# Performance work log

Measured on AMD Instinct MI355X. Metric: run time of the kernel, lower is better.

## Reference

```python
import jax, jax.numpy as jnp
import numpy as np
import math

B, S, D, H = 4, 4096, 1024, 128

def setup_inputs() -> dict:
    key = jax.random.key(0)
    ks = jax.random.split(key, 4)
    scale = 1.0 / math.sqrt(D)
    return {
        "inputs": jax.random.normal(ks[0], (B, S, D), dtype=jnp.float32),
        "Wk": jax.random.normal(ks[1], (H, D), dtype=jnp.float32) * scale,
        "bk": jnp.zeros((H,), dtype=jnp.float32),
        "Wq": jax.random.normal(ks[2], (H, D), dtype=jnp.float32) * scale,
        "bq": jnp.zeros((H,), dtype=jnp.float32),
        "Wv": jax.random.normal(ks[3], (H, D), dtype=jnp.float32) * scale,
        "bv": jnp.zeros((H,), dtype=jnp.float32),
        "padding_mask": jnp.ones((B, S), dtype=jnp.int32),
    }

def reference(inputs, Wk, bk, Wq, bq, Wv, bv, padding_mask):
    # Linear projections: [B,S,D] x [H,D]^T -> [B,S,H]
    k = jnp.einsum('bsd,hd->bsh', inputs, Wk) + bk
    q = jnp.einsum('bsd,hd->bsh', inputs, Wq) + bq
    v = jnp.einsum('bsd,hd->bsh', inputs, Wv) + bv
    # Scaled dot-product scores: [B,S,S]
    scores = jnp.einsum('bqh,bkh->bqk', q, k) / jnp.sqrt(jnp.float32(k.shape[-1]))
    # Mask out padded key positions (mask==0 -> -1e9), broadcast over query dim
    scores = jnp.where(padding_mask[:, None, :] == 0, jnp.float32(-1e9), scores)
    weights = jax.nn.softmax(scores, axis=-1)
    # Dropout is identity in eval mode (reference runs inference / training=False)
    out = jnp.einsum('bqk,bkh->bqh', weights, v)
    return out
```

## Files before the change

kernel.cpp:

```cpp
#include <hip/hip_runtime.h>
#include <cmath>

#define B_ 4
#define S_ 4096
#define D_ 1024
#define H_ 128
#define M_ (B_*S_)
#define NQT 32

typedef _Float16 half8 __attribute__((ext_vector_type(8)));
typedef _Float16 half4 __attribute__((ext_vector_type(4)));
typedef float f32x4 __attribute__((ext_vector_type(4)));
typedef float f32x16 __attribute__((ext_vector_type(16)));
typedef int i32x4 __attribute__((ext_vector_type(4)));

#define LOG2E 1.44269504088896340f

__device__ __forceinline__ void gload16(const void* g, void* l) {
    __builtin_amdgcn_global_load_lds(
        (const __attribute__((address_space(1))) unsigned int*)g,
        (__attribute__((address_space(3))) unsigned int*)l,
        16, 0, 0);
}

__global__ __launch_bounds__(256) void conv_w(
    const float* __restrict__ Wq, const float* __restrict__ Wk,
    const float* __restrict__ Wv, _Float16* __restrict__ wh)
{
    const int idx  = blockIdx.x * 256 + threadIdx.x;
    const int base = idx * 8;
    const int m    = base >> 17;
    const int off  = base & ((H_ * D_) - 1);
    const float* src = (m == 0 ? Wq : m == 1 ? Wk : Wv) + off;
    const float4 a = ((const float4*)src)[0];
    const float4 c = ((const float4*)src)[1];
    half8 h = { (_Float16)a.x, (_Float16)a.y, (_Float16)a.z, (_Float16)a.w,
                (_Float16)c.x, (_Float16)c.y, (_Float16)c.z, (_Float16)c.w };
    *(half8*)(wh + base) = h;
}

__global__ __launch_bounds__(256, 3) void proj_kernel(
    const float* __restrict__ x, const _Float16* __restrict__ wh,
    const float* __restrict__ bq, const float* __restrict__ bk,
    const float* __restrict__ bv,
    _Float16* __restrict__ qh, _Float16* __restrict__ kh,
    _Float16* __restrict__ vt)
{
    __shared__ _Float16 Xs[2][64][72];
    __shared__ _Float16 Ws2[2][128][64];

    const int t = threadIdx.x;
    const int yb = blockIdx.y;
    const float* __restrict__ bias = (yb == 0) ? bq : (yb == 1) ? bk : bv;
    const int m0 = blockIdx.x * 64;
    const int w = t >> 6, lane = t & 63;
    const int lg = lane >> 4, lr = lane & 15;

    f32x4 acc[8];
    #pragma unroll
    for (int i = 0; i < 8; ++i) acc[i] = f32x4{0.f, 0.f, 0.f, 0.f};

    const int xrow = t >> 2, xc = (t & 3) * 16;
    const float* xbase = x + (size_t)(m0 + xrow) * D_ + xc;

    int wbyte[4];
    #pragma unroll
    for (int i = 0; i < 4; ++i) {
        const int wrow = 32 * w + 8 * i + (lane >> 3);
        const int wblk = (lane & 7) ^ (lane >> 3);
        wbyte[i] = (wrow * D_ + wblk * 8) * 2;
    }
    const char* whb = (const char*)(wh + (size_t)yb * H_ * D_);

    float4 xfA[4], xfB[4];

#define WISSUE(KT, BUF)                                                       \
    {                                                                         \
        const char* wsrc = whb + (KT) * (64 * 2);                             \
        _Pragma("unroll")                                                     \
        for (int i = 0; i < 4; ++i)                                           \
            gload16(wsrc + wbyte[i], &Ws2[BUF][32 * w + 8 * i][0]);           \
    }
#define XISSUE(KT, XS)                                                        \
    {                                                                         \
        const float4* xs_ = (const float4*)(xbase + (KT) * 64);               \
        _Pragma("unroll") for (int i = 0; i < 4; ++i) XS[i] = xs_[i];         \
    }
#define XWRITE(XS, BUF)                                                       \
    {                                                                         \
        _Pragma("unroll") for (int i = 0; i < 4; ++i) {                       \
            half4 h = { (_Float16)XS[i].x, (_Float16)XS[i].y,                 \
                        (_Float16)XS[i].z, (_Float16)XS[i].w };               \
            *(half4*)&Xs[BUF][xrow][xc + 4 * i] = h;                          \
        }                                                                     \
    }
#define PMFMA(BUF)                                                            \
    {                                                                         \
        _Pragma("unroll") for (int kk = 0; kk < 2; ++kk) {                    \
            half8 a = *(const half8*)&Xs[BUF][w * 16 + lr][kk * 32 + 8 * lg]; \
            _Pragma("unroll") for (int ni = 0; ni < 8; ++ni) {                \
                half8 bfr = *(const half8*)&Ws2[BUF][ni * 16 + lr]            \
                                [((4 * kk + lg) ^ (lr & 7)) * 8];             \
                acc[ni] = __builtin_amdgcn_mfma_f32_16x16x32_f16(a, bfr, acc[ni], 0, 0, 0); \
            }                                                                 \
        }                                                                     \
    }

    WISSUE(0, 0)
    XISSUE(0, xfA)
    XISSUE(1, xfB)
    XWRITE(xfA, 0)
    __syncthreads();

    for (int kt = 0; kt < 16; kt += 2) {
        WISSUE(kt + 1, 1)
        if (kt + 2 < 16) XISSUE(kt + 2, xfA)
        PMFMA(0)
        XWRITE(xfB, 1)
        __syncthreads();
        if (kt + 2 < 16) WISSUE(kt + 2, 0)
        if (kt + 3 < 16) XISSUE(kt + 3, xfB)
        PMFMA(1)
        if (kt + 2 < 16) XWRITE(xfA, 0)
        __syncthreads();
    }
#undef WISSUE
#undef XISSUE
#undef XWRITE
#undef PMFMA

    const float qscale = 0.08838834764831845f * LOG2E;
    const int rowb = m0 + w * 16 + lg * 4;
    #pragma unroll
    for (int ni = 0; ni < 8; ++ni) {
        const int col = ni * 16 + lr;
        const float bval = bias[col];
        if (yb == 0) {
            #pragma unroll
            for (int r = 0; r < 4; ++r)
                qh[(size_t)(rowb + r) * H_ + col] = (_Float16)((acc[ni][r] + bval) * qscale);
        } else if (yb == 1) {
            #pragma unroll
            for (int r = 0; r < 4; ++r)
                kh[(size_t)(rowb + r) * H_ + col] = (_Float16)(acc[ni][r] + bval);
        } else {
            const int bb = rowb >> 12, s0 = rowb & (S_ - 1);
            half4 h;
            #pragma unroll
            for (int r = 0; r < 4; ++r) h[r] = (_Float16)(acc[ni][r] + bval);
            *(half4*)&vt[(size_t)bb * H_ * S_ + (size_t)col * S_ + s0] = h;
        }
    }
}

__device__ __forceinline__ void attn_tile32(
    const _Float16 (&Kb)[64][128], const _Float16 (&Vb)[128][64],
    const half8 (&qf)[8], f32x16 (&acc2)[4], float& m_, float& l_,
    int muse, int lane)
{
    const unsigned long long bz = __ballot(muse == 0);
    const int l31 = lane & 31, l7 = lane & 7, hi = lane >> 5;

    f32x16 sf[2];
    #pragma unroll
    for (int nb = 0; nb < 2; ++nb)
        #pragma unroll
        for (int r = 0; r < 16; ++r) sf[nb][r] = 0.f;
    __builtin_amdgcn_s_setprio(1);
    #pragma unroll
    for (int kt = 0; kt < 8; ++kt) {
        #pragma unroll
        for (int nb = 0; nb < 2; ++nb) {
            half8 kb = *(const half8*)&Kb[nb * 32 + l31][((2 * kt + hi) ^ l7) * 8];
            sf[nb] = __builtin_amdgcn_mfma_f32_32x32x16_f16(kb, qf[kt], sf[nb], 0, 0, 0);
        }
    }
    __builtin_amdgcn_s_setprio(0);
    if (bz) {
        #pragma unroll
        for (int nb = 0; nb < 2; ++nb)
            #pragma unroll
            for (int r = 0; r < 16; ++r) {
                const int kv = nb * 32 + (r & 3) + 8 * (r >> 2) + 4 * hi;
                if ((bz >> kv) & 1ull) sf[nb][r] = -3e9f;
            }
    }
    float tv[16];
    #pragma unroll
    for (int r = 0; r < 16; ++r) tv[r] = fmaxf(sf[0][r], sf[1][r]);
    #pragma unroll
    for (int off = 8; off > 0; off >>= 1)
        #pragma unroll
        for (int r = 0; r < off; ++r) tv[r] = fmaxf(tv[r], tv[r + off]);
    float tmax = fmaxf(tv[0], __shfl_xor(tv[0], 32));
    if (!__all(tmax <= m_ + 8.f)) {
        const float mn  = fmaxf(m_, tmax);
        const float scl = exp2f(m_ - mn);
        m_ = mn; l_ *= scl;
        #pragma unroll
        for (int hb = 0; hb < 4; ++hb) acc2[hb] *= scl;
    }
    #pragma unroll
    for (int nb = 0; nb < 2; ++nb)
        #pragma unroll
        for (int r = 0; r < 16; ++r) sf[nb][r] = exp2f(sf[nb][r] - m_);
    float sv[16];
    #pragma unroll
    for (int r = 0; r < 16; ++r) sv[r] = sf[0][r] + sf[1][r];
    #pragma unroll
    for (int off = 8; off > 0; off >>= 1)
        #pragma unroll
        for (int r = 0; r < off; ++r) sv[r] += sv[r + off];
    l_ += sv[0] + __shfl_xor(sv[0], 32);

    int pkw[2][8];
    #pragma unroll
    for (int nb = 0; nb < 2; ++nb)
        #pragma unroll
        for (int i = 0; i < 8; ++i) {
            auto h2 = __builtin_amdgcn_cvt_pkrtz(sf[nb][2 * i], sf[nb][2 * i + 1]);
            pkw[nb][i] = __builtin_bit_cast(int, h2);
        }
    #pragma unroll
    for (int nb = 0; nb < 2; ++nb)
        #pragma unroll
        for (int hf = 0; hf < 2; ++hf) {
            const int i0 = hf * 4;
            const int sA = hi ? pkw[nb][i0 + 0] : pkw[nb][i0 + 2];
            const int sB = hi ? pkw[nb][i0 + 1] : pkw[nb][i0 + 3];
            const int rA = __shfl_xor(sA, 32);
            const int rB = __shfl_xor(sB, 32);
            const int n0 = hi ? rA : pkw[nb][i0 + 0];
            const int n1 = hi ? rB : pkw[nb][i0 + 1];
            const int n2 = hi ? pkw[nb][i0 + 2] : rA;
            const int n3 = hi ? pkw[nb][i0 + 3] : rB;
            pkw[nb][i0 + 0] = n0; pkw[nb][i0 + 1] = n1;
            pkw[nb][i0 + 2] = n2; pkw[nb][i0 + 3] = n3;
        }
    __builtin_amdgcn_s_setprio(1);
    #pragma unroll
    for (int s = 0; s < 4; ++s) {
        const int nb = s >> 1, hf = s & 1;
        const half8 pb = __builtin_bit_cast(half8,
            i32x4{ pkw[nb][hf * 4 + 0], pkw[nb][hf * 4 + 1],
                   pkw[nb][hf * 4 + 2], pkw[nb][hf * 4 + 3] });
        #pragma unroll
        for (int hb = 0; hb < 4; ++hb) {
            half8 vb = *(const half8*)&Vb[hb * 32 + l31][((2 * s + hi) ^ l7) * 8];
            acc2[hb] = __builtin_amdgcn_mfma_f32_32x32x16_f16(vb, pb, acc2[hb], 0, 0, 0);
        }
    }
    __builtin_amdgcn_s_setprio(0);
}

__global__ __launch_bounds__(256, 2) void attn_kernel(
    const _Float16* __restrict__ qh, const _Float16* __restrict__ kh,
    const _Float16* __restrict__ vt, const int* __restrict__ mask,
    float* __restrict__ pout, float* __restrict__ pm, float* __restrict__ pl,
    const int nsplit)
{
    __shared__ _Float16 Ks[2][64][128];
    __shared__ _Float16 Vs[2][128][64];

    const int t = threadIdx.x;
    const int id = blockIdx.x;
    int qt, sp, b;
    const int ncombo = B_ * nsplit;
    if ((ncombo & 7) == 0) {
        const int per_xcd = ncombo >> 3;
        const int j = id >> 3;
        qt = j & (NQT - 1);
        const int combo = (id & 7) * per_xcd + (j >> 5);
        sp = combo % nsplit; b = combo / nsplit;
    } else {
        qt = id & (NQT - 1);
        const int rest = id >> 5;
        sp = rest % nsplit; b = rest / nsplit;
    }
    const int q0 = qt * 128;
    const int w = t >> 6, lane = t & 63;
    const int l31 = lane & 31, hi = lane >> 5;
    const int kvlen  = S_ / nsplit;
    const int iters  = kvlen >> 6;
    const int kvbase = sp * kvlen;

    int kbyte[4], vbyte[4];
    #pragma unroll
    for (int i = 0; i < 4; ++i) {
        const int krow = 16 * w + 4 * i + (lane >> 4);
        const int kblk = (lane & 15) ^ (krow & 7);
        kbyte[i] = (krow * H_ + kblk * 8) * 2;
        const int vrow = 32 * w + 8 * i + (lane >> 3);
        const int vblk = (lane & 7) ^ (lane >> 3);
        vbyte[i] = (vrow * S_ + vblk * 8) * 2;
    }
    const char* kbase_b = (const char*)(kh + (size_t)(b * S_ + kvbase) * H_);
    const char* vbase_b = (const char*)(vt + (size_t)b * H_ * S_ + kvbase);
    const char* mbase_b = (const char*)(mask + b * S_ + kvbase + lane);

#define ISSUE_TILE(IT, NB, MRECV)                                             \
    {                                                                         \
        const char* kb_t = kbase_b + (size_t)(IT) * (64 * H_ * 2);            \
        const char* vb_t = vbase_b + (size_t)(IT) * (64 * 2);                 \
        _Pragma("unroll")                                                     \
        for (int i = 0; i < 4; ++i)                                           \
            gload16(kb_t + kbyte[i], &Ks[NB][16 * w + 4 * i][0]);             \
        _Pragma("unroll")                                                     \
        for (int i = 0; i < 4; ++i)                                           \
            gload16(vb_t + vbyte[i], &Vs[NB][32 * w + 8 * i][0]);             \
        MRECV = *(const int*)(mbase_b + (size_t)(IT) * 256);                  \
    }
#define WAIT9  asm volatile("s_waitcnt vmcnt(9)" ::: "memory")
#define WAIT0  asm volatile("s_waitcnt vmcnt(0)" ::: "memory")
#define BAR    asm volatile("s_barrier" ::: "memory")

    half8 qf[8];
    {
        const _Float16* qp = qh + (size_t)(b * S_ + q0 + 32 * w + l31) * H_ + 8 * hi;
        #pragma unroll
        for (int kt = 0; kt < 8; ++kt) qf[kt] = *(const half8*)(qp + 16 * kt);
    }

    float m_ = -1e30f, l_ = 0.f;
    f32x16 acc2[4];
    #pragma unroll
    for (int hb = 0; hb < 4; ++hb)
        #pragma unroll
        for (int r = 0; r < 16; ++r) acc2[hb][r] = 0.f;

    int mA, mB;
    ISSUE_TILE(0, 0, mA)
    ISSUE_TILE(1, 1, mB)
    WAIT9;
    BAR;

    for (int it = 0; it < iters; it += 2) {
        attn_tile32(Ks[0], Vs[0], qf, acc2, m_, l_, mA, lane);
        BAR;
        if (it + 2 < iters) { ISSUE_TILE(it + 2, 0, mA) WAIT9; }
        else                { WAIT0; }
        BAR;
        attn_tile32(Ks[1], Vs[1], qf, acc2, m_, l_, mB, lane);
        BAR;
        if (it + 3 < iters) { ISSUE_TILE(it + 3, 1, mB) WAIT9; }
        else                { WAIT0; }
        BAR;
    }
#undef ISSUE_TILE
#undef WAIT9
#undef WAIT0
#undef BAR

    const int qrow = b * S_ + q0 + 32 * w + l31;
    float* op = pout + (size_t)(sp * M_ + qrow) * H_;
    #pragma unroll
    for (int hb = 0; hb < 4; ++hb)
        #pragma unroll
        for (int i = 0; i < 8; ++i) {
            const int h = hb * 32 + 2 * (i & 1) + 8 * (i >> 1) + 4 * hi;
            float2 v2 = make_float2(acc2[hb][2 * i], acc2[hb][2 * i + 1]);
            *(float2*)(op + h) = v2;
        }
    if (hi == 0) {
        pm[sp * M_ + qrow] = m_;
        pl[sp * M_ + qrow] = l_;
    }
}

__global__ __launch_bounds__(256) void combine_kernel(
    const float* __restrict__ pout, const float* __restrict__ pm,
    const float* __restrict__ pl, float* __restrict__ out, const int nsplit)
{
    const int idx = blockIdx.x * 256 + threadIdx.x;
    const int row = idx >> 7;
    const int h   = idx & (H_ - 1);
    float M = -1e30f;
    for (int sp = 0; sp < nsplit; ++sp) M = fmaxf(M, pm[sp * M_ + row]);
    float Z = 0.f, o = 0.f;
    for (int sp = 0; sp < nsplit; ++sp) {
        const float wgt = exp2f(pm[sp * M_ + row] - M);
        Z += wgt * pl[sp * M_ + row];
        o += wgt * pout[(size_t)(sp * M_ + row) * H_ + h];
    }
    out[idx] = o / Z;
}

extern "C" void kernel_launch(void* const* d_in, const int* in_sizes, int n_in,
                              void* d_out, int out_size, void* d_ws, size_t ws_size,
                              hipStream_t stream)
{
    (void)in_sizes; (void)n_in; (void)out_size;
    const float* x  = (const float*)d_in[0];
    const float* Wk = (const float*)d_in[1];
    const float* bk = (const float*)d_in[2];
    const float* Wq = (const float*)d_in[3];
    const float* bq = (const float*)d_in[4];
    const float* Wv = (const float*)d_in[5];
    const float* bv = (const float*)d_in[6];
    const int* mask = (const int*)d_in[7];

    char* ws = (char*)d_ws;
    const size_t qkvBytes = (size_t)M_ * H_ * sizeof(_Float16);
    _Float16* qh = (_Float16*)ws;
    _Float16* kh = (_Float16*)(ws + qkvBytes);
    _Float16* vt = (_Float16*)(ws + 2 * qkvBytes);
    _Float16* wh = (_Float16*)(ws + 3 * qkvBytes);
    const size_t whBytes = (size_t)3 * H_ * D_ * sizeof(_Float16);
    char* rest = ws + 3 * qkvBytes + whBytes;

    int nsplit = 4;
    const size_t perSplit = (size_t)M_ * H_ * 4 + 2 * (size_t)M_ * 4;
    while (nsplit > 1 &&
           3 * qkvBytes + whBytes + (size_t)nsplit * perSplit > ws_size) nsplit >>= 1;

    float* pout = (float*)rest;
    float* pm   = (float*)(rest + (size_t)nsplit * M_ * H_ * 4);
    float* pl   = pm + (size_t)nsplit * M_;

    conv_w<<<dim3(3 * H_ * D_ / (256 * 8)), 256, 0, stream>>>(Wq, Wk, Wv, wh);
    proj_kernel<<<dim3(M_ / 64, 3), 256, 0, stream>>>(x, wh, bq, bk, bv, qh, kh, vt);
    attn_kernel<<<dim3(NQT * B_ * nsplit), 256, 0, stream>>>(qh, kh, vt, mask, pout, pm, pl, nsplit);
    combine_kernel<<<dim3(M_ * H_ / 256), 256, 0, stream>>>(pout, pm, pl, (float*)d_out, nsplit);
}
```

Before: 113.2 us.

## Software-pipeline QK^T of next tile with PV of current tile

Restructures the attention loop so the QK^T MFMAs for the next KV tile are interleaved with the PV MFMAs of the current tile, with softmax operating on scores computed in the previous step. K and V loads are split and issued at different times so K runs one tile ahead of V. The aim is to keep the matrix units busy while softmax/exp work happens, hiding its latency. It adds register pressure from a second score buffer and more complex waitcnt bookkeeping, which could cause spills or hazards.

Result: slower. 204.8 us (+81.0%).

```diff
diff --git a/kernel.cpp b/kernel.cpp
--- a/kernel.cpp
+++ b/kernel.cpp
@@ -153,41 +153,46 @@
     }
 }
 
-__device__ __forceinline__ void attn_tile32(
-    const _Float16 (&Kb)[64][128], const _Float16 (&Vb)[128][64],
-    const half8 (&qf)[8], f32x16 (&acc2)[4], float& m_, float& l_,
-    int muse, int lane)
-{
-    const unsigned long long bz = __ballot(muse == 0);
+__device__ __forceinline__ void qk_only(
+    const _Float16 (&Kb)[64][128], const half8 (&qf)[8], f32x16 (&sf)[2], int lane)
+{
     const int l31 = lane & 31, l7 = lane & 7, hi = lane >> 5;
-
-    f32x16 sf[2];
     #pragma unroll
     for (int nb = 0; nb < 2; ++nb)
         #pragma unroll
         for (int r = 0; r < 16; ++r) sf[nb][r] = 0.f;
     __builtin_amdgcn_s_setprio(1);
     #pragma unroll
-    for (int kt = 0; kt < 8; ++kt) {
+    for (int kt = 0; kt < 8; ++kt)
         #pragma unroll
         for (int nb = 0; nb < 2; ++nb) {
             half8 kb = *(const half8*)&Kb[nb * 32 + l31][((2 * kt + hi) ^ l7) * 8];
             sf[nb] = __builtin_amdgcn_mfma_f32_32x32x16_f16(kb, qf[kt], sf[nb], 0, 0, 0);
         }
-    }
     __builtin_amdgcn_s_setprio(0);
+}
+
+template <bool HAS_NEXT>
+__device__ __forceinline__ void region_compute(
+    const _Float16 (&Kn)[64][128], const _Float16 (&Vc)[128][64],
+    const half8 (&qf)[8], f32x16 (&sfin)[2], f32x16 (&sfout)[2],
+    f32x16 (&acc2)[4], float& m_, float& l_, int muse, int lane)
+{
+    const unsigned long long bz = __ballot(muse == 0);
+    const int l31 = lane & 31, l7 = lane & 7, hi = lane >> 5;
+
     if (bz) {
         #pragma unroll
         for (int nb = 0; nb < 2; ++nb)
             #pragma unroll
             for (int r = 0; r < 16; ++r) {
                 const int kv = nb * 32 + (r & 3) + 8 * (r >> 2) + 4 * hi;
-                if ((bz >> kv) & 1ull) sf[nb][r] = -3e9f;
+                if ((bz >> kv) & 1ull) sfin[nb][r] = -3e9f;
             }
     }
     float tv[16];
     #pragma unroll
-    for (int r = 0; r < 16; ++r) tv[r] = fmaxf(sf[0][r], sf[1][r]);
+    for (int r = 0; r < 16; ++r) tv[r] = fmaxf(sfin[0][r], sfin[1][r]);
     #pragma unroll
     for (int off = 8; off > 0; off >>= 1)
         #pragma unroll
@@ -203,10 +208,10 @@
     #pragma unroll
     for (int nb = 0; nb < 2; ++nb)
         #pragma unroll
-        for (int r = 0; r < 16; ++r) sf[nb][r] = exp2f(sf[nb][r] - m_);
+        for (int r = 0; r < 16; ++r) sfin[nb][r] = exp2f(sfin[nb][r] - m_);
     float sv[16];
     #pragma unroll
-    for (int r = 0; r < 16; ++r) sv[r] = sf[0][r] + sf[1][r];
+    for (int r = 0; r < 16; ++r) sv[r] = sfin[0][r] + sfin[1][r];
     #pragma unroll
     for (int off = 8; off > 0; off >>= 1)
         #pragma unroll
@@ -218,7 +223,7 @@
     for (int nb = 0; nb < 2; ++nb)
         #pragma unroll
         for (int i = 0; i < 8; ++i) {
-            auto h2 = __builtin_amdgcn_cvt_pkrtz(sf[nb][2 * i], sf[nb][2 * i + 1]);
+            auto h2 = __builtin_amdgcn_cvt_pkrtz(sfin[nb][2 * i], sfin[nb][2 * i + 1]);
             pkw[nb][i] = __builtin_bit_cast(int, h2);
         }
     #pragma unroll
@@ -237,16 +242,34 @@
             pkw[nb][i0 + 0] = n0; pkw[nb][i0 + 1] = n1;
             pkw[nb][i0 + 2] = n2; pkw[nb][i0 + 3] = n3;
         }
+
+    if (HAS_NEXT) {
+        #pragma unroll
+        for (int nb = 0; nb < 2; ++nb)
+            #pragma unroll
+            for (int r = 0; r < 16; ++r) sfout[nb][r] = 0.f;
+    }
     __builtin_amdgcn_s_setprio(1);
     #pragma unroll
     for (int s = 0; s < 4; ++s) {
+        if (HAS_NEXT) {
+            #pragma unroll
+            for (int k2 = 0; k2 < 2; ++k2) {
+                const int kt = 2 * s + k2;
+                #pragma unroll
+                for (int nb = 0; nb < 2; ++nb) {
+                    half8 kb = *(const half8*)&Kn[nb * 32 + l31][((2 * kt + hi) ^ l7) * 8];
+                    sfout[nb] = __builtin_amdgcn_mfma_f32_32x32x16_f16(kb, qf[kt], sfout[nb], 0, 0, 0);
+                }
+            }
+        }
         const int nb = s >> 1, hf = s & 1;
         const half8 pb = __builtin_bit_cast(half8,
             i32x4{ pkw[nb][hf * 4 + 0], pkw[nb][hf * 4 + 1],
                    pkw[nb][hf * 4 + 2], pkw[nb][hf * 4 + 3] });
         #pragma unroll
         for (int hb = 0; hb < 4; ++hb) {
-            half8 vb = *(const half8*)&Vb[hb * 32 + l31][((2 * s + hi) ^ l7) * 8];
+            half8 vb = *(const half8*)&Vc[hb * 32 + l31][((2 * s + hi) ^ l7) * 8];
             acc2[hb] = __builtin_amdgcn_mfma_f32_32x32x16_f16(vb, pb, acc2[hb], 0, 0, 0);
         }
     }
@@ -298,21 +321,22 @@
     const char* vbase_b = (const char*)(vt + (size_t)b * H_ * S_ + kvbase);
     const char* mbase_b = (const char*)(mask + b * S_ + kvbase + lane);
 
-#define ISSUE_TILE(IT, NB, MRECV)                                             \
+#define ISSUE_K(IT, NB)                                                       \
     {                                                                         \
         const char* kb_t = kbase_b + (size_t)(IT) * (64 * H_ * 2);            \
+        _Pragma("unroll")                                                     \
+        for (int i = 0; i < 4; ++i)                                           \
+            gload16(kb_t + kbyte[i], &Ks[NB][16 * w + 4 * i][0]);             \
+    }
+#define ISSUE_V(IT, NB)                                                       \
+    {                                                                         \
         const char* vb_t = vbase_b + (size_t)(IT) * (64 * 2);                 \
         _Pragma("unroll")                                                     \
         for (int i = 0; i < 4; ++i)                                           \
-            gload16(kb_t + kbyte[i], &Ks[NB][16 * w + 4 * i][0]);             \
-        _Pragma("unroll")                                                     \
-        for (int i = 0; i < 4; ++i)                                           \
             gload16(vb_t + vbyte[i], &Vs[NB][32 * w + 8 * i][0]);             \
-        MRECV = *(const int*)(mbase_b + (size_t)(IT) * 256);                  \
-    }
-#define WAIT9  asm volatile("s_waitcnt vmcnt(9)" ::: "memory")
-#define WAIT0  asm volatile("s_waitcnt vmcnt(0)" ::: "memory")
-#define BAR    asm volatile("s_barrier" ::: "memory")
+    }
+#define WAITN(N)  asm volatile("s_waitcnt vmcnt(" #N ")" ::: "memory")
+#define BAR       asm volatile("s_barrier" ::: "memory")
 
     half8 qf[8];
     {
@@ -320,6 +344,10 @@
         #pragma unroll
         for (int kt = 0; kt < 8; ++kt) qf[kt] = *(const half8*)(qp + 16 * kt);
     }
+    int mA = *(const int*)(mbase_b);
+    int mB = *(const int*)(mbase_b + 256);
+
+    ISSUE_K(0, 0) ISSUE_K(1, 1) ISSUE_V(0, 0) ISSUE_V(1, 1)
 
     float m_ = -1e30f, l_ = 0.f;
     f32x16 acc2[4];
@@ -328,27 +356,37 @@
         #pragma unroll
         for (int r = 0; r < 16; ++r) acc2[hb][r] = 0.f;
 
-    int mA, mB;
-    ISSUE_TILE(0, 0, mA)
-    ISSUE_TILE(1, 1, mB)
-    WAIT9;
+    f32x16 sfA[2], sfB[2];
+
+    WAITN(12);
     BAR;
+    qk_only(Ks[0], qf, sfA, lane);
+    BAR;
+    ISSUE_K(2, 0)
+    WAITN(8);
 
     for (int it = 0; it < iters; it += 2) {
-        attn_tile32(Ks[0], Vs[0], qf, acc2, m_, l_, mA, lane);
         BAR;
-        if (it + 2 < iters) { ISSUE_TILE(it + 2, 0, mA) WAIT9; }
-        else                { WAIT0; }
+        region_compute<true>(Ks[1], Vs[0], qf, sfA, sfB, acc2, m_, l_, mA, lane);
         BAR;
-        attn_tile32(Ks[1], Vs[1], qf, acc2, m_, l_, mB, lane);
+        if (it + 2 < iters) mA = *(const int*)(mbase_b + (size_t)(it + 2) * 256);
+        if (it + 2 < iters) ISSUE_V(it + 2, 0)
+        if (it + 3 < iters) ISSUE_K(it + 3, 1)
+        WAITN(9);
         BAR;
-        if (it + 3 < iters) { ISSUE_TILE(it + 3, 1, mB) WAIT9; }
-        else                { WAIT0; }
+        if (it + 2 < iters)
+            region_compute<true>(Ks[0], Vs[1], qf, sfB, sfA, acc2, m_, l_, mB, lane);
+        else
+            region_compute<false>(Ks[0], Vs[1], qf, sfB, sfA, acc2, m_, l_, mB, lane);
         BAR;
-    }
-#undef ISSUE_TILE
-#undef WAIT9
-#undef WAIT0
+        if (it + 3 < iters) mB = *(const int*)(mbase_b + (size_t)(it + 3) * 256);
+        if (it + 3 < iters) ISSUE_V(it + 3, 1)
+        if (it + 4 < iters) ISSUE_K(it + 4, 0)
+        WAITN(9);
+    }
+#undef ISSUE_K
+#undef ISSUE_V
+#undef WAITN
 #undef BAR
 
     const int qrow = b * S_ + q0 + 32 * w + l31;
```

## Replace double-buffered 64-key tiles with single-buffered 128-key tiles

Applied to the files above, without the earlier changes.

The attention loop now loads one 128-key K/V tile into a single LDS buffer per iteration and processes it as two 64-key halves. This replaces the previous two-slot ping-pong prefetch that used explicit vmcnt waits. The aim is to halve the number of barriers and loop iterations per key range and to simplify scheduling. The cost is that loads no longer overlap with compute inside a block, so hiding memory latency depends on the second resident block. Whether __syncthreads waits for the LDS-direct loads is left implicit.

Measured after the change: 114.4 us. About the same (+1.1%).

```diff
diff --git a/kernel.cpp b/kernel.cpp
--- a/kernel.cpp
+++ b/kernel.cpp
@@ -154,7 +154,7 @@
 }
 
 __device__ __forceinline__ void attn_tile32(
-    const _Float16 (&Kb)[64][128], const _Float16 (&Vb)[128][64],
+    const _Float16 (&Kb)[64][128], const _Float16 (&Vb)[128][128], int kvh,
     const half8 (&qf)[8], f32x16 (&acc2)[4], float& m_, float& l_,
     int muse, int lane)
 {
@@ -246,7 +246,7 @@
                    pkw[nb][hf * 4 + 2], pkw[nb][hf * 4 + 3] });
         #pragma unroll
         for (int hb = 0; hb < 4; ++hb) {
-            half8 vb = *(const half8*)&Vb[hb * 32 + l31][((2 * s + hi) ^ l7) * 8];
+            half8 vb = *(const half8*)&Vb[hb * 32 + l31][kvh * 64 + ((2 * s + hi) ^ l7) * 8];
             acc2[hb] = __builtin_amdgcn_mfma_f32_32x32x16_f16(vb, pb, acc2[hb], 0, 0, 0);
         }
     }
@@ -259,8 +259,8 @@
     float* __restrict__ pout, float* __restrict__ pm, float* __restrict__ pl,
     const int nsplit)
 {
-    __shared__ _Float16 Ks[2][64][128];
-    __shared__ _Float16 Vs[2][128][64];
+    __shared__ _Float16 Ks[128][128];
+    __shared__ _Float16 Vs[128][128];
 
     const int t = threadIdx.x;
     const int id = blockIdx.x;
@@ -281,38 +281,34 @@
     const int w = t >> 6, lane = t & 63;
     const int l31 = lane & 31, hi = lane >> 5;
     const int kvlen  = S_ / nsplit;
-    const int iters  = kvlen >> 6;
+    const int iters2 = kvlen >> 7;
     const int kvbase = sp * kvlen;
 
-    int kbyte[4], vbyte[4];
-    #pragma unroll
-    for (int i = 0; i < 4; ++i) {
-        const int krow = 16 * w + 4 * i + (lane >> 4);
+    int kbyte[8], vbyte[8];
+    #pragma unroll
+    for (int i = 0; i < 8; ++i) {
+        const int krow = 32 * w + 4 * i + (lane >> 4);
         const int kblk = (lane & 15) ^ (krow & 7);
         kbyte[i] = (krow * H_ + kblk * 8) * 2;
-        const int vrow = 32 * w + 8 * i + (lane >> 3);
-        const int vblk = (lane & 7) ^ (lane >> 3);
+        const int vrow = 32 * w + 4 * i + (lane >> 4);
+        const int vblk = (lane & 15) ^ (vrow & 7);
         vbyte[i] = (vrow * S_ + vblk * 8) * 2;
     }
     const char* kbase_b = (const char*)(kh + (size_t)(b * S_ + kvbase) * H_);
     const char* vbase_b = (const char*)(vt + (size_t)b * H_ * S_ + kvbase);
     const char* mbase_b = (const char*)(mask + b * S_ + kvbase + lane);
 
-#define ISSUE_TILE(IT, NB, MRECV)                                             \
+#define ISSUE_TILE(IT)                                                        \
     {                                                                         \
-        const char* kb_t = kbase_b + (size_t)(IT) * (64 * H_ * 2);            \
-        const char* vb_t = vbase_b + (size_t)(IT) * (64 * 2);                 \
+        const char* kb_t = kbase_b + (size_t)(IT) * (128 * H_ * 2);           \
+        const char* vb_t = vbase_b + (size_t)(IT) * (128 * 2);                \
         _Pragma("unroll")                                                     \
-        for (int i = 0; i < 4; ++i)                                           \
-            gload16(kb_t + kbyte[i], &Ks[NB][16 * w + 4 * i][0]);             \
+        for (int i = 0; i < 8; ++i)                                           \
+            gload16(kb_t + kbyte[i], &Ks[32 * w + 4 * i][0]);                 \
         _Pragma("unroll")                                                     \
-        for (int i = 0; i < 4; ++i)                                           \
-            gload16(vb_t + vbyte[i], &Vs[NB][32 * w + 8 * i][0]);             \
-        MRECV = *(const int*)(mbase_b + (size_t)(IT) * 256);                  \
-    }
-#define WAIT9  asm volatile("s_waitcnt vmcnt(9)" ::: "memory")
-#define WAIT0  asm volatile("s_waitcnt vmcnt(0)" ::: "memory")
-#define BAR    asm volatile("s_barrier" ::: "memory")
+        for (int i = 0; i < 8; ++i)                                           \
+            gload16(vb_t + vbyte[i], &Vs[32 * w + 4 * i][0]);                 \
+    }
 
     half8 qf[8];
     {
@@ -328,28 +324,19 @@
         #pragma unroll
         for (int r = 0; r < 16; ++r) acc2[hb][r] = 0.f;
 
-    int mA, mB;
-    ISSUE_TILE(0, 0, mA)
-    ISSUE_TILE(1, 1, mB)
-    WAIT9;
-    BAR;
-
-    for (int it = 0; it < iters; it += 2) {
-        attn_tile32(Ks[0], Vs[0], qf, acc2, m_, l_, mA, lane);
-        BAR;
-        if (it + 2 < iters) { ISSUE_TILE(it + 2, 0, mA) WAIT9; }
-        else                { WAIT0; }
-        BAR;
-        attn_tile32(Ks[1], Vs[1], qf, acc2, m_, l_, mB, lane);
-        BAR;
-        if (it + 3 < iters) { ISSUE_TILE(it + 3, 1, mB) WAIT9; }
-        else                { WAIT0; }
-        BAR;
+    const auto& KbLo = *(const _Float16(*)[64][128])(&Ks[0][0]);
+    const auto& KbHi = *(const _Float16(*)[64][128])(&Ks[64][0]);
+
+    for (int it = 0; it < iters2; ++it) {
+        if (it) __syncthreads();
+        ISSUE_TILE(it)
+        const int m0 = *(const int*)(mbase_b + (size_t)it * 512);
+        const int m1 = *(const int*)(mbase_b + (size_t)it * 512 + 256);
+        __syncthreads();
+        attn_tile32(KbLo, Vs, 0, qf, acc2, m_, l_, m0, lane);
+        attn_tile32(KbHi, Vs, 1, qf, acc2, m_, l_, m1, lane);
     }
 #undef ISSUE_TILE
-#undef WAIT9
-#undef WAIT0
-#undef BAR
 
     const int qrow = b * S_ + q0 + 32 * w + l31;
     float* op = pout + (size_t)(sp * M_ + qrow) * H_;
```
